# Kernel optimization log

Measured on AMD Instinct MI355X. Metric: run time of the kernel, lower is better.

## Reference

```python
import jax, jax.numpy as jnp
import numpy as np

GROUP_SIZE = 64
QMAX = 7.0   # int4 symmetric: clamp(round(x/s), -8, 7), zero-point = 0
QMIN = -8.0
EPS = 1e-8


def _group_quant_dequant(t, group_size):
    """Symmetric per-group int4 quantize + dequantize along the last dim.

    t: [..., F] with F % group_size == 0
    Returns dequantized tensor of same shape (equals q_int * scale, which is
    mathematically what the packed int4 GEMM with inline scale dequant computes).
    """
    shp = t.shape
    tg = t.reshape(shp[:-1] + (shp[-1] // group_size, group_size))
    scale = jnp.max(jnp.abs(tg), axis=-1, keepdims=True) / QMAX
    scale = jnp.maximum(scale, EPS)
    q = jnp.clip(jnp.round(tg / scale), QMIN, QMAX)
    return (q * scale).reshape(shp)


def setup_inputs() -> dict:
    key = jax.random.key(0)
    k1, k2 = jax.random.split(key)
    x = jax.random.normal(k1, (8192, 4096), dtype=jnp.float32)
    weight = jax.random.normal(k2, (4096, 4096), dtype=jnp.float32) * 0.02
    return {"x": x, "weight": weight}


def reference(x, weight):
    # ActQuantizerGS: per-token, per-group-of-64 symmetric int4 quant of x.
    x_dq = _group_quant_dequant(x, GROUP_SIZE)          # [T, K]
    # WeightQuantizer + LinearFLHGS: per-(out_channel, group) symmetric int4
    # weight quant; GEMM with inline scale dequant. Because scales are constant
    # within each group, int-accumulate-then-scale == dequant-then-matmul.
    w_dq = _group_quant_dequant(weight, GROUP_SIZE)     # [O, K]
    return x_dq @ w_dq.T                                # [T, O]
```

## Files before the change

### kernel.cpp

```cpp
#include <hip/hip_runtime.h>
#include <hip/hip_bf16.h>
#include <stdint.h>


typedef __bf16 bf16x8 __attribute__((ext_vector_type(8)));
typedef float f32x4 __attribute__((ext_vector_type(4)));

static __device__ __forceinline__ uint16_t f32_to_bf16_rne(float f) {
    uint32_t u = __float_as_uint(f);
    uint32_t r = (u + 0x7fffu + ((u >> 16) & 1u)) >> 16;
    return (uint16_t)r;
}

__global__ void quant_kernel(const float* __restrict__ in,
                             uint16_t* __restrict__ out, int total4) {
    int nthreads = gridDim.x * blockDim.x;
    int t = blockIdx.x * blockDim.x + threadIdx.x;
    for (int i = t; i < total4; i += nthreads) {
        float4 v = ((const float4*)in)[i];
        float amax = fmaxf(fmaxf(fabsf(v.x), fabsf(v.y)),
                           fmaxf(fabsf(v.z), fabsf(v.w)));
        #pragma unroll
        for (int m = 1; m <= 8; m <<= 1)
            amax = fmaxf(amax, __shfl_xor(amax, m, 64));
        float s = fmaxf(amax * (1.0f / 7.0f), 1e-8f);
        float q0 = fminf(fmaxf(rintf(v.x / s), -8.0f), 7.0f);
        float q1 = fminf(fmaxf(rintf(v.y / s), -8.0f), 7.0f);
        float q2 = fminf(fmaxf(rintf(v.z / s), -8.0f), 7.0f);
        float q3 = fminf(fmaxf(rintf(v.w / s), -8.0f), 7.0f);
        ushort4 o;
        o.x = f32_to_bf16_rne(q0 * s);
        o.y = f32_to_bf16_rne(q1 * s);
        o.z = f32_to_bf16_rne(q2 * s);
        o.w = f32_to_bf16_rne(q3 * s);
        ((ushort4*)out)[i] = o;
    }
}

#define BM 256
#define BN 256
#define BK 64

__global__ __launch_bounds__(512, 2) void gemm8_kernel(
        const uint16_t* __restrict__ A, const uint16_t* __restrict__ B,
        float* __restrict__ C, int M, int N, int K) {
    __shared__ uint16_t As[2][2][128 * 64];
    __shared__ uint16_t Bs[2][2][128 * 64];

    const int NTt = K >> 6;

    int nwg = gridDim.x;
    int bid = blockIdx.x;
    int swz = bid;
    if ((nwg & 7) == 0) {
        int cpx = nwg >> 3;
        swz = (bid & 7) * cpx + (bid >> 3);
    }
    int nbn = N / BN;
    int bm = swz / nbn, bn = swz % nbn;

    int tid = threadIdx.x;
    int lane = tid & 63;
    int wid = tid >> 6;
    int wm = wid >> 2;
    int wn = wid & 3;

    const int rowA0 = bm * BM;
    const int colB0 = bn * BN;

    int srow = lane >> 3;
    int scol = ((lane & 7) ^ (lane >> 3)) << 3;

    int rl = lane & 15;
    int cg = lane >> 4;
    int coff[2];
    coff[0] = ((0 + cg) ^ (rl & 7)) << 3;
    coff[1] = ((4 + cg) ^ (rl & 7)) << 3;

    f32x4 acc[8][4] = {};

    auto stageA = [&](int buf, int half, int t) {
        #pragma unroll
        for (int j = 0; j < 2; ++j) {
            int rowin = wid * 16 + j * 8;
            const uint16_t* g = A + (size_t)(rowA0 + half * 128 + rowin + srow) * K
                                  + t * 64 + scol;
            uint16_t* l = &As[buf][half][rowin * 64];
            __builtin_amdgcn_global_load_lds(
                (const __attribute__((address_space(1))) void*)g,
                (__attribute__((address_space(3))) void*)l, 16, 0, 0);
        }
    };
    auto stageB = [&](int buf, int half, int t) {
        #pragma unroll
        for (int j = 0; j < 2; ++j) {
            int rowin = wid * 16 + j * 8;
            const uint16_t* g = B + (size_t)(colB0 + half * 128 + rowin + srow) * K
                                  + t * 64 + scol;
            uint16_t* l = &Bs[buf][half][rowin * 64];
            __builtin_amdgcn_global_load_lds(
                (const __attribute__((address_space(1))) void*)g,
                (__attribute__((address_space(3))) void*)l, 16, 0, 0);
        }
    };

    stageA(0, 0, 0); stageA(0, 1, 0);
    stageB(0, 0, 0); stageB(0, 1, 0);
    if (NTt > 1) {
        stageB(1, 0, 1); stageB(1, 1, 1);
        asm volatile("s_waitcnt vmcnt(4)" ::: "memory");
    } else {
        asm volatile("s_waitcnt vmcnt(0)" ::: "memory");
    }
    asm volatile("" ::: "memory");
    __builtin_amdgcn_s_barrier();
    asm volatile("" ::: "memory");

    bf16x8 aLo[4][2], aHi[4][2], bLo[2][2], bHi[2][2];
    const int bhalf = wn >> 1;
    const int brow0 = (wn & 1) * 64;

#define PHASE_MID() \
    asm volatile("" ::: "memory"); \
    __builtin_amdgcn_s_barrier(); \
    asm volatile("s_waitcnt lgkmcnt(0)" ::: "memory"); \
    __builtin_amdgcn_sched_barrier(0); \
    __builtin_amdgcn_s_setprio(1);

#define PHASE_END() \
    __builtin_amdgcn_s_setprio(0); \
    asm volatile("" ::: "memory"); \
    __builtin_amdgcn_s_barrier(); \
    asm volatile("" ::: "memory");

    for (int t = 0; t < NTt; ++t) {
        int cb = t & 1, nb = cb ^ 1;

        #pragma unroll
        for (int mi = 0; mi < 4; ++mi)
            #pragma unroll
            for (int ks = 0; ks < 2; ++ks)
                aLo[mi][ks] = *(const bf16x8*)&As[cb][wm][(mi * 16 + rl) * 64 + coff[ks]];
        #pragma unroll
        for (int ni = 0; ni < 2; ++ni)
            #pragma unroll
            for (int ks = 0; ks < 2; ++ks)
                bLo[ni][ks] = *(const bf16x8*)&Bs[cb][bhalf][(brow0 + ni * 16 + rl) * 64 + coff[ks]];
        if (t + 1 < NTt) stageA(nb, 0, t + 1);
        PHASE_MID();
        #pragma unroll
        for (int mi = 0; mi < 4; ++mi)
            #pragma unroll
            for (int ni = 0; ni < 2; ++ni)
                #pragma unroll
                for (int ks = 0; ks < 2; ++ks)
                    acc[mi][ni] = __builtin_amdgcn_mfma_f32_16x16x32_bf16(
                        aLo[mi][ks], bLo[ni][ks], acc[mi][ni], 0, 0, 0);
        PHASE_END();

        #pragma unroll
        for (int ni = 0; ni < 2; ++ni)
            #pragma unroll
            for (int ks = 0; ks < 2; ++ks)
                bHi[ni][ks] = *(const bf16x8*)&Bs[cb][bhalf][(brow0 + (ni + 2) * 16 + rl) * 64 + coff[ks]];
        if (t + 1 < NTt) stageA(nb, 1, t + 1);
        PHASE_MID();
        #pragma unroll
        for (int mi = 0; mi < 4; ++mi)
            #pragma unroll
            for (int ni = 0; ni < 2; ++ni)
                #pragma unroll
                for (int ks = 0; ks < 2; ++ks)
                    acc[mi][ni + 2] = __builtin_amdgcn_mfma_f32_16x16x32_bf16(
                        aLo[mi][ks], bHi[ni][ks], acc[mi][ni + 2], 0, 0, 0);
        PHASE_END();

        #pragma unroll
        for (int mi = 0; mi < 4; ++mi)
            #pragma unroll
            for (int ks = 0; ks < 2; ++ks)
                aHi[mi][ks] = *(const bf16x8*)&As[cb][wm][((mi + 4) * 16 + rl) * 64 + coff[ks]];
        if (t + 2 < NTt) stageB(cb, 0, t + 2);
        PHASE_MID();
        #pragma unroll
        for (int mi = 0; mi < 4; ++mi)
            #pragma unroll
            for (int ni = 0; ni < 2; ++ni)
                #pragma unroll
                for (int ks = 0; ks < 2; ++ks)
                    acc[mi + 4][ni] = __builtin_amdgcn_mfma_f32_16x16x32_bf16(
                        aHi[mi][ks], bLo[ni][ks], acc[mi + 4][ni], 0, 0, 0);
        PHASE_END();

        if (t + 2 < NTt) stageB(cb, 1, t + 2);
        asm volatile("" ::: "memory");
        __builtin_amdgcn_s_barrier();
        __builtin_amdgcn_sched_barrier(0);
        __builtin_amdgcn_s_setprio(1);
        #pragma unroll
        for (int mi = 0; mi < 4; ++mi)
            #pragma unroll
            for (int ni = 0; ni < 2; ++ni)
                #pragma unroll
                for (int ks = 0; ks < 2; ++ks)
                    acc[mi + 4][ni + 2] = __builtin_amdgcn_mfma_f32_16x16x32_bf16(
                        aHi[mi][ks], bHi[ni][ks], acc[mi + 4][ni + 2], 0, 0, 0);
        __builtin_amdgcn_s_setprio(0);
        if (t + 2 < NTt) asm volatile("s_waitcnt vmcnt(4)" ::: "memory");
        else             asm volatile("s_waitcnt vmcnt(0)" ::: "memory");
        asm volatile("" ::: "memory");
        __builtin_amdgcn_s_barrier();
        asm volatile("" ::: "memory");
    }

    int cl = lane & 15;
    int rq = (lane >> 4) * 4;
    #pragma unroll
    for (int mi = 0; mi < 8; ++mi) {
        #pragma unroll
        for (int ni = 0; ni < 4; ++ni) {
            int row = rowA0 + wm * 128 + mi * 16 + rq;
            int col = colB0 + wn * 64 + ni * 16 + cl;
            float* cp = C + (size_t)row * N + col;
            #pragma unroll
            for (int r = 0; r < 4; ++r)
                cp[(size_t)r * N] = acc[mi][ni][r];
        }
    }
#undef PHASE_MID
#undef PHASE_END
}

extern "C" void kernel_launch(void* const* d_in, const int* in_sizes, int n_in,
                              void* d_out, int out_size, void* d_ws, size_t ws_size,
                              hipStream_t stream) {
    const float* x = (const float*)d_in[0];
    const float* w = (const float*)d_in[1];
    float* out = (float*)d_out;

    const int K = 4096;
    const int T = in_sizes[0] / K;
    const int O = in_sizes[1] / K;

    uint16_t* xq = (uint16_t*)d_ws;
    uint16_t* wq = (uint16_t*)((char*)d_ws + (size_t)T * K * 2);

    quant_kernel<<<2048, 256, 0, stream>>>(x, xq, (T * K) >> 2);
    quant_kernel<<<2048, 256, 0, stream>>>(w, wq, (O * K) >> 2);

    int nwg = (T / BM) * (O / BN);
    gemm8_kernel<<<nwg, 512, 0, stream>>>(xq, wq, out, T, O, K);
}
```

Before: 306.2 us.

## Restructure GEMM pipeline: load all fragments upfront, prefetch full tile two ahead

The GEMM main loop is reorganised from four barrier-separated phases, each with its own LDS fragment load and partial global stage, into a single block. All A/B fragments for the current K tile are read from LDS up front. Global loads for tile t+2 (both A and B) are issued after one mid-loop barrier, and the prologue now preloads two full tiles. This cuts the per-iteration barriers from about seven to two and gives the loads more time to land. The cost is higher register pressure from holding all fragments at once, and less interleaving of LDS reads with MFMAs.

```diff
diff --git a/kernel.cpp b/kernel.cpp
--- a/kernel.cpp
+++ b/kernel.cpp
@@ -41,7 +41,9 @@
 #define BN 256
 #define BK 64
 
-__global__ __launch_bounds__(512, 2) void gemm8_kernel(
+#define FENCE() asm volatile("" ::: "memory")
+
+__global__ __launch_bounds__(512, 2) void gemm_kernel(
         const uint16_t* __restrict__ A, const uint16_t* __restrict__ B,
         float* __restrict__ C, int M, int N, int K) {
     __shared__ uint16_t As[2][2][128 * 64];
@@ -107,35 +109,22 @@
     stageA(0, 0, 0); stageA(0, 1, 0);
     stageB(0, 0, 0); stageB(0, 1, 0);
     if (NTt > 1) {
+        stageA(1, 0, 1); stageA(1, 1, 1);
         stageB(1, 0, 1); stageB(1, 1, 1);
-        asm volatile("s_waitcnt vmcnt(4)" ::: "memory");
+        asm volatile("s_waitcnt vmcnt(8)" ::: "memory");
     } else {
         asm volatile("s_waitcnt vmcnt(0)" ::: "memory");
     }
-    asm volatile("" ::: "memory");
-    __builtin_amdgcn_s_barrier();
-    asm volatile("" ::: "memory");
-
-    bf16x8 aLo[4][2], aHi[4][2], bLo[2][2], bHi[2][2];
+    FENCE(); __builtin_amdgcn_s_barrier(); FENCE();
+
     const int bhalf = wn >> 1;
     const int brow0 = (wn & 1) * 64;
 
-#define PHASE_MID() \
-    asm volatile("" ::: "memory"); \
-    __builtin_amdgcn_s_barrier(); \
-    asm volatile("s_waitcnt lgkmcnt(0)" ::: "memory"); \
-    __builtin_amdgcn_sched_barrier(0); \
-    __builtin_amdgcn_s_setprio(1);
-
-#define PHASE_END() \
-    __builtin_amdgcn_s_setprio(0); \
-    asm volatile("" ::: "memory"); \
-    __builtin_amdgcn_s_barrier(); \
-    asm volatile("" ::: "memory");
-
     for (int t = 0; t < NTt; ++t) {
-        int cb = t & 1, nb = cb ^ 1;
-
+        int cb = t & 1;
+        const bool more = (t + 2 < NTt);
+
+        bf16x8 aLo[4][2], bLo[2][2], bHi[2][2], aHi[4][2];
         #pragma unroll
         for (int mi = 0; mi < 4; ++mi)
             #pragma unroll
@@ -146,8 +135,18 @@
             #pragma unroll
             for (int ks = 0; ks < 2; ++ks)
                 bLo[ni][ks] = *(const bf16x8*)&Bs[cb][bhalf][(brow0 + ni * 16 + rl) * 64 + coff[ks]];
-        if (t + 1 < NTt) stageA(nb, 0, t + 1);
-        PHASE_MID();
+        #pragma unroll
+        for (int ni = 0; ni < 2; ++ni)
+            #pragma unroll
+            for (int ks = 0; ks < 2; ++ks)
+                bHi[ni][ks] = *(const bf16x8*)&Bs[cb][bhalf][(brow0 + (ni + 2) * 16 + rl) * 64 + coff[ks]];
+        #pragma unroll
+        for (int mi = 0; mi < 4; ++mi)
+            #pragma unroll
+            for (int ks = 0; ks < 2; ++ks)
+                aHi[mi][ks] = *(const bf16x8*)&As[cb][wm][((mi + 4) * 16 + rl) * 64 + coff[ks]];
+
+        __builtin_amdgcn_s_setprio(1);
         #pragma unroll
         for (int mi = 0; mi < 4; ++mi)
             #pragma unroll
@@ -156,15 +155,9 @@
                 for (int ks = 0; ks < 2; ++ks)
                     acc[mi][ni] = __builtin_amdgcn_mfma_f32_16x16x32_bf16(
                         aLo[mi][ks], bLo[ni][ks], acc[mi][ni], 0, 0, 0);
-        PHASE_END();
-
-        #pragma unroll
-        for (int ni = 0; ni < 2; ++ni)
-            #pragma unroll
-            for (int ks = 0; ks < 2; ++ks)
-                bHi[ni][ks] = *(const bf16x8*)&Bs[cb][bhalf][(brow0 + (ni + 2) * 16 + rl) * 64 + coff[ks]];
-        if (t + 1 < NTt) stageA(nb, 1, t + 1);
-        PHASE_MID();
+        __builtin_amdgcn_s_setprio(0);
+
+        __builtin_amdgcn_s_setprio(1);
         #pragma unroll
         for (int mi = 0; mi < 4; ++mi)
             #pragma unroll
@@ -173,15 +166,9 @@
                 for (int ks = 0; ks < 2; ++ks)
                     acc[mi][ni + 2] = __builtin_amdgcn_mfma_f32_16x16x32_bf16(
                         aLo[mi][ks], bHi[ni][ks], acc[mi][ni + 2], 0, 0, 0);
-        PHASE_END();
-
-        #pragma unroll
-        for (int mi = 0; mi < 4; ++mi)
-            #pragma unroll
-            for (int ks = 0; ks < 2; ++ks)
-                aHi[mi][ks] = *(const bf16x8*)&As[cb][wm][((mi + 4) * 16 + rl) * 64 + coff[ks]];
-        if (t + 2 < NTt) stageB(cb, 0, t + 2);
-        PHASE_MID();
+        __builtin_amdgcn_s_setprio(0);
+
+        __builtin_amdgcn_s_setprio(1);
         #pragma unroll
         for (int mi = 0; mi < 4; ++mi)
             #pragma unroll
@@ -190,12 +177,16 @@
                 for (int ks = 0; ks < 2; ++ks)
                     acc[mi + 4][ni] = __builtin_amdgcn_mfma_f32_16x16x32_bf16(
                         aHi[mi][ks], bLo[ni][ks], acc[mi + 4][ni], 0, 0, 0);
-        PHASE_END();
-
-        if (t + 2 < NTt) stageB(cb, 1, t + 2);
-        asm volatile("" ::: "memory");
-        __builtin_amdgcn_s_barrier();
+        __builtin_amdgcn_s_setprio(0);
+
+        FENCE(); __builtin_amdgcn_s_barrier(); FENCE();
+
+        if (more) {
+            stageA(cb, 0, t + 2); stageA(cb, 1, t + 2);
+            stageB(cb, 0, t + 2); stageB(cb, 1, t + 2);
+        }
         __builtin_amdgcn_sched_barrier(0);
+
         __builtin_amdgcn_s_setprio(1);
         #pragma unroll
         for (int mi = 0; mi < 4; ++mi)
@@ -206,11 +197,10 @@
                     acc[mi + 4][ni + 2] = __builtin_amdgcn_mfma_f32_16x16x32_bf16(
                         aHi[mi][ks], bHi[ni][ks], acc[mi + 4][ni + 2], 0, 0, 0);
         __builtin_amdgcn_s_setprio(0);
-        if (t + 2 < NTt) asm volatile("s_waitcnt vmcnt(4)" ::: "memory");
-        else             asm volatile("s_waitcnt vmcnt(0)" ::: "memory");
-        asm volatile("" ::: "memory");
-        __builtin_amdgcn_s_barrier();
-        asm volatile("" ::: "memory");
+
+        if (more) asm volatile("s_waitcnt vmcnt(8)" ::: "memory");
+        else      asm volatile("s_waitcnt vmcnt(0)" ::: "memory");
+        FENCE(); __builtin_amdgcn_s_barrier(); FENCE();
     }
 
     int cl = lane & 15;
@@ -227,8 +217,6 @@
                 cp[(size_t)r * N] = acc[mi][ni][r];
         }
     }
-#undef PHASE_MID
-#undef PHASE_END
 }
 
 extern "C" void kernel_launch(void* const* d_in, const int* in_sizes, int n_in,
@@ -249,5 +237,5 @@
     quant_kernel<<<2048, 256, 0, stream>>>(w, wq, (O * K) >> 2);
 
     int nwg = (T / BM) * (O / BN);
-    gemm8_kernel<<<nwg, 512, 0, stream>>>(xq, wq, out, T, O, K);
-}
+    gemm_kernel<<<nwg, 512, 0, stream>>>(xq, wq, out, T, O, K);
+}
```

Result: faster. 299.6 us (-2.2%).
